# Kernel tuning notes

Measured on AMD Instinct MI355X. Metric: run time of the kernel, lower is better.

The kernel has to match this reference:

```python
import jax, jax.numpy as jnp
import numpy as np

ALPHA = 0.5  # learn_alpha=False -> constant

def _init(key, shape, fan_in):
    return jax.random.normal(key, shape, dtype=jnp.float32) / np.sqrt(fan_in)

def setup_inputs() -> dict:
    key = jax.random.key(0)
    ks = jax.random.split(key, 12)
    B, S, N, F, H, E = 4, 8, 4000, 64, 128, 32000
    x_seq = jax.random.normal(ks[0], (B, S, N, F), dtype=jnp.float32)
    edge_index = jax.random.randint(ks[1], (B, S, 2, E), 0, N, dtype=jnp.int32)
    edge_weight = jax.random.uniform(ks[2], (B, S, E), dtype=jnp.float32)
    params = dict(
        W0_s=_init(ks[3], (H, F), F), b0_s=jnp.zeros((H,), jnp.float32),
        W0_d=_init(ks[4], (H, F), F), b0_d=jnp.zeros((H,), jnp.float32),
        W1_s=_init(ks[5], (H, H), H), b1_s=jnp.zeros((H,), jnp.float32),
        W1_d=_init(ks[6], (H, H), H), b1_d=jnp.zeros((H,), jnp.float32),
        lstm_Wih=_init(ks[7], (4 * H, H), H), lstm_Whh=_init(ks[8], (4 * H, H), H),
        lstm_bih=jnp.zeros((4 * H,), jnp.float32), lstm_bhh=jnp.zeros((4 * H,), jnp.float32),
        Wp=_init(ks[9], (F, H), H), bp=jnp.zeros((F,), jnp.float32),
    )
    return {"x_seq": x_seq, "edge_index": edge_index, "edge_weight": edge_weight, **params}

def _dir_gcn(x, src, dst, ew, Ws, bs, Wd, bd):
    # x: [N, Fin]. DirGCN: alpha * W_s(A_hat x) + (1-alpha) * W_d(A_hat^T x)
    # with symmetric directed normalization D_out^{-1/2} A D_in^{-1/2}.
    N = x.shape[0]
    deg_out = jax.ops.segment_sum(ew, src, num_segments=N)
    deg_in = jax.ops.segment_sum(ew, dst, num_segments=N)
    inv_out = jnp.where(deg_out > 0, jax.lax.rsqrt(jnp.maximum(deg_out, 1e-12)), 0.0)
    inv_in = jnp.where(deg_in > 0, jax.lax.rsqrt(jnp.maximum(deg_in, 1e-12)), 0.0)
    norm = ew * inv_out[src] * inv_in[dst]                         # [E]
    agg_f = jax.ops.segment_sum(norm[:, None] * x[src], dst, num_segments=N)  # A_hat x
    agg_b = jax.ops.segment_sum(norm[:, None] * x[dst], src, num_segments=N)  # A_hat^T x
    return ALPHA * (agg_f @ Ws.T + bs) + (1.0 - ALPHA) * (agg_b @ Wd.T + bd)

def reference(x_seq, edge_index, edge_weight, W0_s, b0_s, W0_d, b0_d,
              W1_s, b1_s, W1_d, b1_d, lstm_Wih, lstm_Whh, lstm_bih, lstm_bhh, Wp, bp):
    B, S, N, F = x_seq.shape
    H = W0_s.shape[0]
    G = B * S
    # fuse the per-(batch, timestep) python loops into one batched graph pass
    x = x_seq.reshape(G, N, F)
    src = edge_index[:, :, 0, :].reshape(G, -1)
    dst = edge_index[:, :, 1, :].reshape(G, -1)
    ew = edge_weight.reshape(G, -1)
    conv = jax.vmap(_dir_gcn, in_axes=(0, 0, 0, 0, None, None, None, None))
    h = conv(x, src, dst, ew, W0_s, b0_s, W0_d, b0_d)   # dropout is a no-op in eval mode
    h = conv(h, src, dst, ew, W1_s, b1_s, W1_d, b1_d)   # [G, N, H]
    # faithful to original: [B, S*N, H].reshape(B*N, S, H) (order-preserving flatten)
    seq = h.reshape(B * N, S, H)
    # single-layer unidirectional LSTM, batch_first; pytorch gate order i,f,g,o
    def step(carry, x_t):
        hprev, c = carry
        gates = x_t @ lstm_Wih.T + lstm_bih + hprev @ lstm_Whh.T + lstm_bhh
        i, f, g, o = jnp.split(gates, 4, axis=-1)
        c = jax.nn.sigmoid(f) * c + jax.nn.sigmoid(i) * jnp.tanh(g)
        hn = jax.nn.sigmoid(o) * jnp.tanh(c)
        return (hn, c), None
    h0 = jnp.zeros((B * N, H), x_seq.dtype)
    (h_last, _), _ = jax.lax.scan(step, (h0, h0), seq.transpose(1, 0, 2))
    return h_last.reshape(B, N, H) @ Wp.T + bp           # [B, N, num_features]
```

## Files before the change

kernel.cpp:

```cpp
#include <hip/hip_runtime.h>
#include <hip/hip_bf16.h>

#define B_  4
#define S_  8
#define N_  4000
#define F_  64
#define H_  128
#define E_  32000
#define G_  (B_*S_)
#define GN_ (G_*N_)
#define M_  (B_*N_)
#define GE_ (G_*E_)
#define HALF_GN 64000
#define HALF_M  8000
#define NBLK_   8
#define EPB_    (E_/NBLK_)

#define OFF_W0S 0
#define OFF_B0S 8192
#define OFF_W0D 8320
#define OFF_B0D 16512
#define OFF_W1S 16640
#define OFF_B1S 33024
#define OFF_W1D 33152
#define OFF_B1D 49536
#define OFF_WIH 49664
#define OFF_WHH 115200
#define OFF_BIH 180736
#define OFF_BHH 181248
#define OFF_WP  181760
#define OFF_BP  189952
#define WCV_TOTAL 190016

#define WS_FLAG   0
#define WS_WCV    16
#define WS_WPH    190032
#define WS_WPC    222800
#define WS_BIASC  288336
#define WS_DEGO   288848
#define WS_DEGI   416848
#define WS_CNTI   544848
#define WS_CNTO   672848
#define WS_RPI    800848
#define WS_RPO    928880
#define WS_CURI   1056912
#define WS_CURO   1184912
#define WS_CSRI   1312912
#define WS_CSRO   3360912
#define WS_X2     5408912
#define WS_PART   9608912
#define WS_HB     21792912
#define WS_GT     29984912
#define WS_WC0    46368912

typedef __attribute__((ext_vector_type(8))) short bf16x8;
typedef __attribute__((ext_vector_type(4))) float f32x4;
typedef __attribute__((ext_vector_type(8))) unsigned short ushort8;

__device__ inline float bfu2f(unsigned short u){ union{unsigned int i; float f;} v; v.i=((unsigned int)u)<<16; return v.f; }
__device__ inline unsigned short f2bfu(float f){ __hip_bfloat16 b = __float2bfloat16(f); return *(unsigned short*)&b; }
__device__ inline float rcpf(float x){ return __builtin_amdgcn_rcpf(x); }
__device__ inline float sigmf(float x){ return rcpf(1.0f + __expf(-x)); }
__device__ inline float tanhfast(float x){ return 1.0f - 2.0f*rcpf(1.0f + __expf(2.0f*x)); }
__device__ inline float loadf(const void* p, long i, int isf32){
    return isf32 ? ((const float*)p)[i]
                 : __bfloat162float(((const __hip_bfloat16*)p)[i]);
}
__device__ inline float4 cvtbf4(ushort4 u){
    float4 f;
    f.x = __uint_as_float(((unsigned)u.x)<<16);
    f.y = __uint_as_float(((unsigned)u.y)<<16);
    f.z = __uint_as_float(((unsigned)u.z)<<16);
    f.w = __uint_as_float(((unsigned)u.w)<<16);
    return f;
}

__global__ void sniff_kernel(const unsigned int* __restrict__ ew, int* __restrict__ flag){
    __shared__ int s;
    if (threadIdx.x == 0) s = 0;
    __syncthreads();
    unsigned int lo = ew[threadIdx.x] & 0xFFFFu;
    if (lo > 0x3F80u) atomicOr(&s, 1);
    __syncthreads();
    if (threadIdx.x == 0) flag[0] = s;
}

struct WSeg { const void* src; int base; int n; };
struct WDesc { WSeg seg[14]; };
__global__ void convert_weights(WDesc d, float* __restrict__ dst, const int* __restrict__ flag){
    int isf32 = flag[0];
    int idx = blockIdx.x*256 + threadIdx.x;
    #pragma unroll
    for (int s=0;s<14;s++){
        int off = idx - d.seg[s].base;
        if (off >= 0 && off < d.seg[s].n){
            dst[idx] = loadf(d.seg[s].src, off, isf32);
            return;
        }
    }
}

__global__ void repack_whh(const float* __restrict__ wcv, unsigned short* __restrict__ whb){
    int idx = blockIdx.x*256 + threadIdx.x;
    whb[idx] = f2bfu(wcv[OFF_WHH + idx]);
}

__global__ void repack_wc0(const float* __restrict__ wcv, unsigned short* __restrict__ wc0){
    int idx = blockIdx.x*256 + threadIdx.x;
    int k = idx & 127, n = idx >> 7;
    float v = (k < 64) ? 0.5f*wcv[OFF_W0S + n*64 + k] : 0.5f*wcv[OFF_W0D + n*64 + (k-64)];
    wc0[idx] = f2bfu(v);
}

__global__ void xcvt_kernel(const void* __restrict__ x, const int* __restrict__ flag,
                            unsigned short* __restrict__ Xb){
    long idx = (long)blockIdx.x*256 + threadIdx.x;
    if (idx >= (long)GN_*64) return;
    Xb[idx] = f2bfu(loadf(x, idx, flag[0]));
}

__global__ __launch_bounds__(256) void compose_wc(const float* __restrict__ wcv,
                                                  unsigned short* __restrict__ wpc){
    int n = blockIdx.x;
    int k = threadIdx.x;
    const float* wih = wcv + OFF_WIH + n*128;
    const float* w1  = (k < 128) ? (wcv + OFF_W1S + k) : (wcv + OFF_W1D + (k-128));
    float s = 0.f;
    for (int h=0; h<128; h++) s += wih[h] * w1[h*128];
    wpc[n*256 + k] = f2bfu(0.5f * s);
}

__global__ void compose_bias(const float* __restrict__ wcv, float* __restrict__ biasc){
    int n = blockIdx.x*256 + threadIdx.x;
    if (n >= 512) return;
    float s = wcv[OFF_BIH+n] + wcv[OFF_BHH+n];
    const float* wih = wcv + OFF_WIH + n*128;
    for (int h=0; h<128; h++) s += wih[h] * 0.5f*(wcv[OFF_B1S+h] + wcv[OFF_B1D+h]);
    biasc[n] = s;
}

__global__ __launch_bounds__(1024) void hist_kernel(
        const int* __restrict__ ei, const void* __restrict__ ew, const int* __restrict__ flag,
        float* __restrict__ part){
    __shared__ float wdo[N_], wdi[N_];
    __shared__ int   co[N_],  ci[N_];
    int xcd  = blockIdx.x & 7;
    int r2   = blockIdx.x >> 3;
    int g    = xcd*4 + (r2 & 3);
    int b    = r2 >> 2;
    int tid  = threadIdx.x;
    int isf32 = flag[0];
    for (int i=tid;i<N_;i+=1024){ wdo[i]=0.f; wdi[i]=0.f; co[i]=0; ci[i]=0; }
    __syncthreads();
    const int* eib = ei + g*2*E_;
    int e0 = b*EPB_;
    for (int e=e0+tid; e<e0+EPB_; e+=1024){
        int s = eib[e], d = eib[E_+e];
        float w = loadf(ew, (long)g*E_+e, isf32);
        atomicAdd(&wdo[s], w); atomicAdd(&wdi[d], w);
        atomicAdd(&co[s], 1);  atomicAdd(&ci[d], 1);
    }
    __syncthreads();
    float* Pdo = part + (size_t)(0*G_ + g)*NBLK_*N_ + (size_t)b*N_;
    float* Pdi = part + (size_t)(1*G_ + g)*NBLK_*N_ + (size_t)b*N_;
    int*   Pci = (int*)part + (size_t)(2*G_ + g)*NBLK_*N_ + (size_t)b*N_;
    int*   Pco = (int*)part + (size_t)(3*G_ + g)*NBLK_*N_ + (size_t)b*N_;
    for (int i=tid;i<N_;i+=1024){
        Pdo[i] = wdo[i]; Pdi[i] = wdi[i];
        Pci[i] = ci[i];  Pco[i] = co[i];
    }
}

__global__ __launch_bounds__(256) void reduce_hist(
        float* __restrict__ part,
        float* __restrict__ deg_o, float* __restrict__ deg_i,
        int* __restrict__ cnt_in, int* __restrict__ cnt_out){
    int g = blockIdx.x >> 4;
    int n = (blockIdx.x & 15)*256 + threadIdx.x;
    if (n >= N_) return;
    float* Pdo = part + (size_t)(0*G_ + g)*NBLK_*N_;
    float* Pdi = part + (size_t)(1*G_ + g)*NBLK_*N_;
    int*   Pci = (int*)part + (size_t)(2*G_ + g)*NBLK_*N_;
    int*   Pco = (int*)part + (size_t)(3*G_ + g)*NBLK_*N_;
    float sdo = 0.f, sdi = 0.f;
    int sci = 0, sco = 0;
    #pragma unroll
    for (int b=0;b<NBLK_;b++){
        size_t idx = (size_t)b*N_ + n;
        sdo += Pdo[idx]; sdi += Pdi[idx];
        int vi = Pci[idx], vo = Pco[idx];
        Pci[idx] = sci;  Pco[idx] = sco;
        sci += vi; sco += vo;
    }
    deg_o[g*N_+n] = sdo; deg_i[g*N_+n] = sdi;
    cnt_in[g*N_+n] = sci; cnt_out[g*N_+n] = sco;
}

__global__ __launch_bounds__(256) void scan_kernel(
        const int* __restrict__ cnt_in, const int* __restrict__ cnt_out,
        int* __restrict__ rp_in, int* __restrict__ rp_out){
    __shared__ int part[256], pref[256];
    int g = blockIdx.x & 31, dir = blockIdx.x >> 5;
    const int* cnt = (dir ? cnt_out : cnt_in) + g*N_;
    int* rp  = (dir ? rp_out  : rp_in)  + g*(N_+1);
    int tid = threadIdx.x, base = tid*16;
    int sum = 0;
    for (int i=0;i<16;i++){ int p = base+i; if (p < N_) sum += cnt[p]; }
    part[tid] = sum;
    __syncthreads();
    if (tid == 0){ int run = 0; for (int j=0;j<256;j++){ pref[j] = run; run += part[j]; } }
    __syncthreads();
    int run = pref[tid];
    for (int i=0;i<16;i++){
        int p = base+i;
        if (p < N_){ rp[p] = run; run += cnt[p]; }
    }
    if (tid == 255) rp[N_] = run;
}

__global__ __launch_bounds__(1024) void fill_kernel(
        const int* __restrict__ ei, const void* __restrict__ ew,
        const int* __restrict__ flag,
        const float* __restrict__ deg_o, const float* __restrict__ deg_i,
        const int* __restrict__ rp_in, const int* __restrict__ rp_out,
        const float* __restrict__ part,
        int2* __restrict__ csr_in, int2* __restrict__ csr_out){
    __shared__ int lci[N_], lco[N_];
    int xcd  = blockIdx.x & 7;
    int r2   = blockIdx.x >> 3;
    int g    = xcd*4 + (r2 & 3);
    int b    = r2 >> 2;
    int tid  = threadIdx.x;
    int isf32 = flag[0];
    for (int i=tid;i<N_;i+=1024){ lci[i]=0; lco[i]=0; }
    __syncthreads();
    const int* eib = ei + g*2*E_;
    const int* cumI = (const int*)part + (size_t)(2*G_ + g)*NBLK_*N_ + (size_t)b*N_;
    const int* cumO = (const int*)part + (size_t)(3*G_ + g)*NBLK_*N_ + (size_t)b*N_;
    const int* rpi = rp_in  + g*(N_+1);
    const int* rpo = rp_out + g*(N_+1);
    int2* ci = csr_in  + (long)g*E_;
    int2* co = csr_out + (long)g*E_;
    int e0 = b*EPB_;
    for (int e=e0+tid; e<e0+EPB_; e+=1024){
        int s = eib[e], d = eib[E_+e];
        float dout = deg_o[g*N_+s], din = deg_i[g*N_+d];
        float io = dout > 0.f ? rsqrtf(fmaxf(dout, 1e-12f)) : 0.f;
        float ii = din  > 0.f ? rsqrtf(fmaxf(din , 1e-12f)) : 0.f;
        float nrm = loadf(ew, (long)g*E_ + e, isf32) * io * ii;
        int li = atomicAdd(&lci[d], 1);
        ci[rpi[d] + cumI[d] + li] = make_int2(s, __float_as_int(nrm));
        int lo = atomicAdd(&lco[s], 1);
        co[rpo[s] + cumO[s] + lo] = make_int2(d, __float_as_int(nrm));
    }
}

__global__ __launch_bounds__(256) void gather64(
        const int* __restrict__ rp_in, const int* __restrict__ rp_out,
        const int2* __restrict__ csr_in, const int2* __restrict__ csr_out,
        const unsigned short* __restrict__ Xb,
        unsigned short* __restrict__ PQ0){
    int xcd  = blockIdx.x & 7;
    int rest = blockIdx.x >> 3;
    int g    = xcd*4 + (rest & 3);
    int chunk= rest >> 2;
    int wave = threadIdx.x >> 6;
    int lane = threadIdx.x & 63;
    int sub  = lane >> 3;
    int li   = lane & 7;
    int wl   = chunk*32 + wave*8 + sub;
    int dir  = wl >= N_;  int n = wl - dir*N_;
    const int*  rp  = (dir ? rp_out : rp_in) + g*(N_+1);
    const int2* csr = (dir ? csr_out : csr_in) + (long)g*E_;
    int pb = rp[n], pe = rp[n+1];
    int plast = max(pe - 1, 0);
    const unsigned short* base = Xb + (size_t)g*N_*64;
    float acc[8];
    #pragma unroll
    for (int j=0;j<8;j++) acc[j] = 0.f;
    for (int p = pb; __any(p < pe); p += 4){
        float w[4]; ushort8 v[4];
        #pragma unroll
        for (int i=0;i<4;i++){
            int pi = p+i;
            int2 ent = csr[min(pi, plast)];
            w[i] = (pi < pe) ? __int_as_float(ent.y) : 0.f;
            v[i] = *(const ushort8*)(base + ent.x*64 + li*8);
        }
        #pragma unroll
        for (int i=0;i<4;i++)
            #pragma unroll
            for (int j=0;j<8;j++)
                acc[j] += w[i]*bfu2f(v[i][j]);
    }
    ushort8 o;
    #pragma unroll
    for (int j=0;j<8;j++) o[j] = f2bfu(acc[j]);
    *(ushort8*)(PQ0 + (size_t)(g*N_+n)*128 + dir*64 + li*8) = o;
}

__global__ __launch_bounds__(256) void gather128(
        const int* __restrict__ rp_in, const int* __restrict__ rp_out,
        const int2* __restrict__ csr_in, const int2* __restrict__ csr_out,
        const unsigned short* __restrict__ hb,
        unsigned short* __restrict__ X2){
    int xcd  = blockIdx.x & 7;
    int rest = blockIdx.x >> 3;
    int g    = xcd*4 + (rest & 3);
    int chunk= rest >> 2;
    int wave = threadIdx.x >> 6;
    int lane = threadIdx.x & 63;
    int sub  = lane >> 4;
    int li   = lane & 15;
    int wl   = chunk*16 + wave*4 + sub;
    int dir  = wl >= N_;  int n = wl - dir*N_;
    const int*  rp  = (dir ? rp_out : rp_in) + g*(N_+1);
    const int2* csr = (dir ? csr_out : csr_in) + (long)g*E_;
    int pb = rp[n], pe = rp[n+1];
    int plast = max(pe - 1, 0);
    const unsigned short* base = hb + (size_t)g*N_*128;
    float acc[8];
    #pragma unroll
    for (int j=0;j<8;j++) acc[j] = 0.f;
    for (int p = pb; __any(p < pe); p += 4){
        float w[4]; ushort8 v[4];
        #pragma unroll
        for (int i=0;i<4;i++){
            int pi = p+i;
            int2 ent = csr[min(pi, plast)];
            w[i] = (pi < pe) ? __int_as_float(ent.y) : 0.f;
            v[i] = *(const ushort8*)(base + ent.x*128 + li*8);
        }
        #pragma unroll
        for (int i=0;i<4;i++)
            #pragma unroll
            for (int j=0;j<8;j++)
                acc[j] += w[i]*bfu2f(v[i][j]);
    }
    ushort8 o;
    #pragma unroll
    for (int j=0;j<8;j++) o[j] = f2bfu(acc[j]);
    *(ushort8*)(X2 + (size_t)(g*N_+n)*256 + dir*128 + li*8) = o;
}

__global__ __launch_bounds__(256) void gemm0(
        const unsigned short* __restrict__ PQ0, const unsigned short* __restrict__ wc0,
        const float* __restrict__ wcv, __hip_bfloat16* __restrict__ Hb){
    __shared__ unsigned short As[2][64*40];
    int tid  = threadIdx.x;
    int wave = tid >> 6, lane = tid & 63;
    int quad = lane >> 4, l16 = lane & 15;
    int nb = blockIdx.x & 1, mb = blockIdx.x >> 1;
    int m0 = mb*64;
    int col = nb*64 + wave*16 + l16;
    bf16x8 bq[4];
    #pragma unroll
    for (int ks=0; ks<4; ks++)
        bq[ks] = *(const bf16x8*)(wc0 + (size_t)col*128 + ks*32 + quad*8);
    f32x4 acc[4];
    #pragma unroll
    for (int t=0;t<4;t++) acc[t] = (f32x4){0.f,0.f,0.f,0.f};
    int srow = tid>>2, sch = tid&3;
    const unsigned short* src_base = PQ0 + (size_t)(m0 + srow)*128 + sch*8;
    *(float4*)(&As[0][srow*40 + sch*8]) = *(const float4*)(src_base);
    __syncthreads();
    for (int ks=0; ks<4; ks++){
        if (ks < 3)
            *(float4*)(&As[(ks+1)&1][srow*40 + sch*8]) = *(const float4*)(src_base + (ks+1)*32);
        const unsigned short* ab = As[ks&1];
        #pragma unroll
        for (int t=0;t<4;t++){
            bf16x8 a = *(const bf16x8*)(ab + (t*16 + l16)*40 + quad*8);
            acc[t] = __builtin_amdgcn_mfma_f32_16x16x32_bf16(a, bq[ks], acc[t], 0, 0, 0);
        }
        __syncthreads();
    }
    float bias = 0.5f*(wcv[OFF_B0S+col] + wcv[OFF_B0D+col]);
    #pragma unroll
    for (int t=0;t<4;t++){
        #pragma unroll
        for (int r=0;r<4;r++){
            int grow = m0 + t*16 + quad*4 + r;
            Hb[(size_t)grow*128 + col] = __float2bfloat16(acc[t][r] + bias);
        }
    }
}

__global__ __launch_bounds__(256) void gemmg(
        const unsigned short* __restrict__ X2, const unsigned short* __restrict__ wpc,
        const float* __restrict__ biasc, unsigned short* __restrict__ gates, int gn_base){
    __shared__ unsigned short As[2][64*40];
    int tid  = threadIdx.x;
    int wave = tid >> 6, lane = tid & 63;
    int quad = lane >> 4, l16 = lane & 15;
    int nb = blockIdx.x & 7, mb = blockIdx.x >> 3;
    int m0 = mb*64;
    int col = nb*64 + wave*16 + l16;
    bf16x8 bq[8];
    #pragma unroll
    for (int ks=0; ks<8; ks++)
        bq[ks] = *(const bf16x8*)(wpc + (size_t)col*256 + ks*32 + quad*8);
    f32x4 acc[4];
    #pragma unroll
    for (int t=0;t<4;t++) acc[t] = (f32x4){0.f,0.f,0.f,0.f};
    int srow = tid>>2, sch = tid&3;
    const unsigned short* src_base = X2 + (size_t)(gn_base + m0 + srow)*256 + sch*8;
    *(float4*)(&As[0][srow*40 + sch*8]) = *(const float4*)(src_base);
    __syncthreads();
    for (int ks=0; ks<8; ks++){
        if (ks < 7)
            *(float4*)(&As[(ks+1)&1][srow*40 + sch*8]) = *(const float4*)(src_base + (ks+1)*32);
        const unsigned short* ab = As[ks&1];
        #pragma unroll
        for (int t=0;t<4;t++){
            bf16x8 a = *(const bf16x8*)(ab + (t*16 + l16)*40 + quad*8);
            acc[t] = __builtin_amdgcn_mfma_f32_16x16x32_bf16(a, bq[ks], acc[t], 0, 0, 0);
        }
        __syncthreads();
    }
    float bc = biasc[col];
    #pragma unroll
    for (int t=0;t<4;t++){
        #pragma unroll
        for (int r=0;r<4;r++){
            int grow = m0 + t*16 + quad*4 + r;
            gates[(size_t)(grow>>3)*4096 + (size_t)col*8 + (grow&7)] = f2bfu(acc[t][r] + bc);
        }
    }
}

__global__ __launch_bounds__(512) void lstm7(
        const unsigned short* __restrict__ gates3, int mbase,
        const unsigned short* __restrict__ whb,
        const float* __restrict__ wcv, const int* __restrict__ flag,
        void* __restrict__ out){
    __shared__ unsigned short hsh[16*136];
    int tid  = threadIdx.x;
    int w    = tid >> 6;
    int lane = tid & 63;
    int quad = lane >> 4, l15 = lane & 15;
    int mlb  = blockIdx.x * 16;
    int m0   = mbase + mlb;
    int isf32 = flag[0];

    ushort8 pg[4][4];
    const unsigned short* gb = gates3 + (size_t)mlb*4096 + (size_t)(w*16 + l15)*8;
    #pragma unroll
    for (int g=0; g<4; g++)
        #pragma unroll
        for (int r=0; r<4; r++)
            pg[g][r] = *(const ushort8*)(gb + (size_t)(quad*4+r)*4096 + (size_t)g*1024);

    bf16x8 bfrag[4][4];
    #pragma unroll
    for (int g=0; g<4; g++)
        #pragma unroll
        for (int kt=0; kt<4; kt++)
            bfrag[g][kt] = *(const bf16x8*)(whb + (size_t)(g*128 + w*16 + l15)*128 + kt*32 + quad*8);

    for (int t=tid; t<16*136; t+=512) hsh[t] = 0;
    f32x4 c = (f32x4){0.f,0.f,0.f,0.f};
    __syncthreads();

    #pragma unroll
    for (int step=0; step<8; step++){
        f32x4 acc[4];
        #pragma unroll
        for (int g=0; g<4; g++)
            #pragma unroll
            for (int r=0; r<4; r++)
                acc[g][r] = bfu2f(pg[g][r][step]);
        #pragma unroll
        for (int kt=0; kt<4; kt++){
            bf16x8 a = *(const bf16x8*)(hsh + l15*136 + kt*32 + quad*8);
            #pragma unroll
            for (int g=0; g<4; g++)
                acc[g] = __builtin_amdgcn_mfma_f32_16x16x32_bf16(a, bfrag[g][kt], acc[g], 0, 0, 0);
        }
        float hnew[4];
        #pragma unroll
        for (int r=0; r<4; r++){
            float gi = sigmf(acc[0][r]), gf = sigmf(acc[1][r]);
            float gg = tanhfast(acc[2][r]), go = sigmf(acc[3][r]);
            float cc = gf*c[r] + gi*gg;
            c[r] = cc;
            hnew[r] = go*tanhfast(cc);
        }
        __syncthreads();
        #pragma unroll
        for (int r=0; r<4; r++)
            hsh[(quad*4+r)*136 + w*16 + l15] = f2bfu(hnew[r]);
        __syncthreads();
    }
    int r  = tid >> 5;
    int q0 = (tid & 31) * 2;
    float p0 = wcv[OFF_BP + q0], p1 = wcv[OFF_BP + q0 + 1];
    for (int k4=0;k4<32;k4++){
        float4 hv = cvtbf4(*(const ushort4*)(hsh + r*136 + k4*4));
        float4 w0 = *(const float4*)(wcv + OFF_WP + q0*128 + k4*4);
        float4 w1 = *(const float4*)(wcv + OFF_WP + (q0+1)*128 + k4*4);
        p0 += w0.x*hv.x + w0.y*hv.y + w0.z*hv.z + w0.w*hv.w;
        p1 += w1.x*hv.x + w1.y*hv.y + w1.z*hv.z + w1.w*hv.w;
    }
    long o = (long)(m0+r)*64 + q0;
    if (isf32){ ((float*)out)[o] = p0; ((float*)out)[o+1] = p1; }
    else { ((__hip_bfloat16*)out)[o] = __float2bfloat16(p0);
           ((__hip_bfloat16*)out)[o+1] = __float2bfloat16(p1); }
}

extern "C" void kernel_launch(void* const* d_in, const int* in_sizes, int n_in,
                              void* d_out, int out_size, void* d_ws, size_t ws_size,
                              hipStream_t stream){
    const void* x_seq      = d_in[0];
    const int*  edge_index = (const int*)d_in[1];
    const void* edge_weight= d_in[2];

    float* ws    = (float*)d_ws;
    int*   flag  = (int*)(ws + WS_FLAG);
    float* wcv   = ws + WS_WCV;
    unsigned short* whb = (unsigned short*)(ws + WS_WPH);
    unsigned short* wpc = (unsigned short*)(ws + WS_WPC);
    unsigned short* wc0 = (unsigned short*)(ws + WS_WC0);
    float* biasc = ws + WS_BIASC;
    float* deg_o = ws + WS_DEGO;
    float* deg_i = ws + WS_DEGI;
    int*   cnt_i = (int*)(ws + WS_CNTI);
    int*   cnt_o = (int*)(ws + WS_CNTO);
    int*   rp_i  = (int*)(ws + WS_RPI);
    int*   rp_o  = (int*)(ws + WS_RPO);
    float* partb = ws + WS_PART;
    int2*  csr_i = (int2*)(ws + WS_CSRI);
    int2*  csr_o = (int2*)(ws + WS_CSRO);
    unsigned short* X2 = (unsigned short*)(ws + WS_X2);
    unsigned short* Xb = X2;
    __hip_bfloat16* Hb = (__hip_bfloat16*)(ws + WS_HB);
    unsigned short* GT = (unsigned short*)(ws + WS_GT);
    unsigned short* PQ0 = GT;

    sniff_kernel<<<1, 256, 0, stream>>>((const unsigned int*)edge_weight, flag);
    WDesc wd;
    wd.seg[0]  = { d_in[3],  OFF_W0S, 8192  };
    wd.seg[1]  = { d_in[4],  OFF_B0S, 128   };
    wd.seg[2]  = { d_in[5],  OFF_W0D, 8192  };
    wd.seg[3]  = { d_in[6],  OFF_B0D, 128   };
    wd.seg[4]  = { d_in[7],  OFF_W1S, 16384 };
    wd.seg[5]  = { d_in[8],  OFF_B1S, 128   };
    wd.seg[6]  = { d_in[9],  OFF_W1D, 16384 };
    wd.seg[7]  = { d_in[10], OFF_B1D, 128   };
    wd.seg[8]  = { d_in[11], OFF_WIH, 65536 };
    wd.seg[9]  = { d_in[12], OFF_WHH, 65536 };
    wd.seg[10] = { d_in[13], OFF_BIH, 512   };
    wd.seg[11] = { d_in[14], OFF_BHH, 512   };
    wd.seg[12] = { d_in[15], OFF_WP,  8192  };
    wd.seg[13] = { d_in[16], OFF_BP,  64    };
    convert_weights<<<(WCV_TOTAL+255)/256, 256, 0, stream>>>(wd, wcv, flag);
    repack_whh<<<256, 256, 0, stream>>>(wcv, whb);
    repack_wc0<<<64, 256, 0, stream>>>(wcv, wc0);
    compose_wc<<<512, 256, 0, stream>>>(wcv, wpc);
    compose_bias<<<2, 256, 0, stream>>>(wcv, biasc);
    xcvt_kernel<<<(GN_*64+255)/256, 256, 0, stream>>>(x_seq, flag, Xb);

    hist_kernel<<<G_*NBLK_, 1024, 0, stream>>>(edge_index, edge_weight, flag, partb);
    reduce_hist<<<G_*16, 256, 0, stream>>>(partb, deg_o, deg_i, cnt_i, cnt_o);
    scan_kernel<<<64, 256, 0, stream>>>(cnt_i, cnt_o, rp_i, rp_o);
    fill_kernel<<<G_*NBLK_, 1024, 0, stream>>>(edge_index, edge_weight, flag,
                                               deg_o, deg_i, rp_i, rp_o, partb, csr_i, csr_o);

    gather64<<<2*G_*N_/32, 256, 0, stream>>>(rp_i, rp_o, csr_i, csr_o, Xb, PQ0);
    gemm0<<<2*(GN_/64), 256, 0, stream>>>(PQ0, wc0, wcv, Hb);

    gather128<<<2*G_*N_/16, 256, 0, stream>>>(rp_i, rp_o, csr_i, csr_o,
                                              (const unsigned short*)Hb, X2);

    gemmg<<<8*(HALF_GN/64), 256, 0, stream>>>(X2, wpc, biasc, GT, 0);
    lstm7<<<HALF_M/16, 512, 0, stream>>>(GT, 0, whb, wcv, flag, d_out);

    gemmg<<<8*(HALF_GN/64), 256, 0, stream>>>(X2, wpc, biasc, GT, HALF_GN);
    lstm7<<<HALF_M/16, 512, 0, stream>>>(GT, HALF_M, whb, wcv, flag, d_out);
}
```

Before: 550.6 us.

## Fuse sparse gathers with following GEMMs via shared-memory tiles

Merges the layer-0 gather and its GEMM into one kernel, and likewise the layer-1 gather and the LSTM input-gate GEMM. Each block aggregates 64 rows for both directions into LDS and then runs MFMA on them directly. This removes the PQ0 and X2 round trips through global memory and two kernel launches. In exchange, each block now serialises gather work before its MFMA phase. The gate kernel recomputes the four column slabs per block with fewer blocks, and load balancing across irregular degrees may suffer.

```diff
diff --git a/kernel.cpp b/kernel.cpp
--- a/kernel.cpp
+++ b/kernel.cpp
@@ -43,8 +43,6 @@
 #define WS_CNTO   672848
 #define WS_RPI    800848
 #define WS_RPO    928880
-#define WS_CURI   1056912
-#define WS_CURO   1184912
 #define WS_CSRI   1312912
 #define WS_CSRO   3360912
 #define WS_X2     5408912
@@ -255,177 +253,163 @@
     }
 }
 
-__global__ __launch_bounds__(256) void gather64(
+__global__ __launch_bounds__(256) void g0fused(
         const int* __restrict__ rp_in, const int* __restrict__ rp_out,
         const int2* __restrict__ csr_in, const int2* __restrict__ csr_out,
-        const unsigned short* __restrict__ Xb,
-        unsigned short* __restrict__ PQ0){
+        const unsigned short* __restrict__ Xb, const unsigned short* __restrict__ wc0,
+        const float* __restrict__ wcv, __hip_bfloat16* __restrict__ Hb){
+    __shared__ unsigned short As[64*136];
     int xcd  = blockIdx.x & 7;
-    int rest = blockIdx.x >> 3;
-    int g    = xcd*4 + (rest & 3);
-    int chunk= rest >> 2;
-    int wave = threadIdx.x >> 6;
-    int lane = threadIdx.x & 63;
-    int sub  = lane >> 3;
-    int li   = lane & 7;
-    int wl   = chunk*32 + wave*8 + sub;
-    int dir  = wl >= N_;  int n = wl - dir*N_;
-    const int*  rp  = (dir ? rp_out : rp_in) + g*(N_+1);
-    const int2* csr = (dir ? csr_out : csr_in) + (long)g*E_;
-    int pb = rp[n], pe = rp[n+1];
-    int plast = max(pe - 1, 0);
-    const unsigned short* base = Xb + (size_t)g*N_*64;
-    float acc[8];
-    #pragma unroll
-    for (int j=0;j<8;j++) acc[j] = 0.f;
-    for (int p = pb; __any(p < pe); p += 4){
-        float w[4]; ushort8 v[4];
-        #pragma unroll
-        for (int i=0;i<4;i++){
-            int pi = p+i;
-            int2 ent = csr[min(pi, plast)];
-            w[i] = (pi < pe) ? __int_as_float(ent.y) : 0.f;
-            v[i] = *(const ushort8*)(base + ent.x*64 + li*8);
+    int tile = blockIdx.x >> 3;
+    int m0   = (xcd*250 + tile)*64;
+    int tid  = threadIdx.x;
+
+    int gid = tid >> 3, li = tid & 7;
+    #pragma unroll
+    for (int t=0; t<4; t++){
+        int task = t*32 + gid;
+        int dir  = task >> 6, r = task & 63;
+        int grow = m0 + r;
+        int g = grow / N_;  int n = grow - g*N_;
+        const int*  rp  = (dir ? rp_out : rp_in) + g*(N_+1);
+        const int2* csr = (dir ? csr_out : csr_in) + (long)g*E_;
+        int pb = rp[n], pe = rp[n+1];
+        int plast = max(pe - 1, 0);
+        const unsigned short* base = Xb + (size_t)g*N_*64;
+        float acc[8];
+        #pragma unroll
+        for (int j=0;j<8;j++) acc[j] = 0.f;
+        for (int p=pb; p<pe; p+=4){
+            float w4[4]; ushort8 v4[4];
+            #pragma unroll
+            for (int i=0;i<4;i++){
+                int pi = p+i;
+                int2 ent = csr[min(pi, plast)];
+                w4[i] = (pi < pe) ? __int_as_float(ent.y) : 0.f;
+                v4[i] = *(const ushort8*)(base + ent.x*64 + li*8);
+            }
+            #pragma unroll
+            for (int i=0;i<4;i++)
+                #pragma unroll
+                for (int j=0;j<8;j++)
+                    acc[j] += w4[i]*bfu2f(v4[i][j]);
         }
-        #pragma unroll
-        for (int i=0;i<4;i++)
-            #pragma unroll
-            for (int j=0;j<8;j++)
-                acc[j] += w[i]*bfu2f(v[i][j]);
-    }
-    ushort8 o;
-    #pragma unroll
-    for (int j=0;j<8;j++) o[j] = f2bfu(acc[j]);
-    *(ushort8*)(PQ0 + (size_t)(g*N_+n)*128 + dir*64 + li*8) = o;
-}
-
-__global__ __launch_bounds__(256) void gather128(
+        ushort8 o;
+        #pragma unroll
+        for (int j=0;j<8;j++) o[j] = f2bfu(acc[j]);
+        *(ushort8*)(&As[r*136 + dir*64 + li*8]) = o;
+    }
+    __syncthreads();
+
+    int wave = tid >> 6, lane = tid & 63;
+    int quad = lane >> 4, l16 = lane & 15;
+    int colb = wave*16 + l16;
+    bf16x8 bq[2][4];
+    f32x4 acc[2][4];
+    #pragma unroll
+    for (int s=0;s<2;s++){
+        #pragma unroll
+        for (int ks=0;ks<4;ks++)
+            bq[s][ks] = *(const bf16x8*)(wc0 + (size_t)(colb + s*64)*128 + ks*32 + quad*8);
+        #pragma unroll
+        for (int t=0;t<4;t++) acc[s][t] = (f32x4){0.f,0.f,0.f,0.f};
+    }
+    #pragma unroll
+    for (int ks=0;ks<4;ks++){
+        #pragma unroll
+        for (int t=0;t<4;t++){
+            bf16x8 a = *(const bf16x8*)(&As[(t*16 + l16)*136 + ks*32 + quad*8]);
+            acc[0][t] = __builtin_amdgcn_mfma_f32_16x16x32_bf16(a, bq[0][ks], acc[0][t], 0, 0, 0);
+            acc[1][t] = __builtin_amdgcn_mfma_f32_16x16x32_bf16(a, bq[1][ks], acc[1][t], 0, 0, 0);
+        }
+    }
+    #pragma unroll
+    for (int s=0;s<2;s++){
+        int col = colb + s*64;
+        float bias = 0.5f*(wcv[OFF_B0S+col] + wcv[OFF_B0D+col]);
+        #pragma unroll
+        for (int t=0;t<4;t++)
+            #pragma unroll
+            for (int r=0;r<4;r++)
+                Hb[(size_t)(m0 + t*16 + quad*4 + r)*128 + col] = __float2bfloat16(acc[s][t][r] + bias);
+    }
+}
+
+__global__ __launch_bounds__(512) void ggfused(
         const int* __restrict__ rp_in, const int* __restrict__ rp_out,
         const int2* __restrict__ csr_in, const int2* __restrict__ csr_out,
         const unsigned short* __restrict__ hb,
-        unsigned short* __restrict__ X2){
+        const unsigned short* __restrict__ wpc, const float* __restrict__ biasc,
+        unsigned short* __restrict__ gates, int gn_base){
+    __shared__ unsigned short As[64*264];
     int xcd  = blockIdx.x & 7;
-    int rest = blockIdx.x >> 3;
-    int g    = xcd*4 + (rest & 3);
-    int chunk= rest >> 2;
-    int wave = threadIdx.x >> 6;
-    int lane = threadIdx.x & 63;
-    int sub  = lane >> 4;
-    int li   = lane & 15;
-    int wl   = chunk*16 + wave*4 + sub;
-    int dir  = wl >= N_;  int n = wl - dir*N_;
-    const int*  rp  = (dir ? rp_out : rp_in) + g*(N_+1);
-    const int2* csr = (dir ? csr_out : csr_in) + (long)g*E_;
-    int pb = rp[n], pe = rp[n+1];
-    int plast = max(pe - 1, 0);
-    const unsigned short* base = hb + (size_t)g*N_*128;
-    float acc[8];
-    #pragma unroll
-    for (int j=0;j<8;j++) acc[j] = 0.f;
-    for (int p = pb; __any(p < pe); p += 4){
-        float w[4]; ushort8 v[4];
-        #pragma unroll
-        for (int i=0;i<4;i++){
-            int pi = p+i;
-            int2 ent = csr[min(pi, plast)];
-            w[i] = (pi < pe) ? __int_as_float(ent.y) : 0.f;
-            v[i] = *(const ushort8*)(base + ent.x*128 + li*8);
+    int tile = blockIdx.x >> 3;
+    int m0   = (xcd*125 + tile)*64;
+    int tid  = threadIdx.x;
+
+    int gid = tid >> 4, li = tid & 15;
+    #pragma unroll
+    for (int t=0; t<4; t++){
+        int task = t*32 + gid;
+        int dir  = task >> 6, r = task & 63;
+        int grow = gn_base + m0 + r;
+        int g = grow / N_;  int n = grow - g*N_;
+        const int*  rp  = (dir ? rp_out : rp_in) + g*(N_+1);
+        const int2* csr = (dir ? csr_out : csr_in) + (long)g*E_;
+        int pb = rp[n], pe = rp[n+1];
+        int plast = max(pe - 1, 0);
+        const unsigned short* base = hb + (size_t)g*N_*128;
+        float acc[8];
+        #pragma unroll
+        for (int j=0;j<8;j++) acc[j] = 0.f;
+        for (int p=pb; p<pe; p+=4){
+            float w4[4]; ushort8 v4[4];
+            #pragma unroll
+            for (int i=0;i<4;i++){
+                int pi = p+i;
+                int2 ent = csr[min(pi, plast)];
+                w4[i] = (pi < pe) ? __int_as_float(ent.y) : 0.f;
+                v4[i] = *(const ushort8*)(base + ent.x*128 + li*8);
+            }
+            #pragma unroll
+            for (int i=0;i<4;i++)
+                #pragma unroll
+                for (int j=0;j<8;j++)
+                    acc[j] += w4[i]*bfu2f(v4[i][j]);
         }
-        #pragma unroll
-        for (int i=0;i<4;i++)
-            #pragma unroll
-            for (int j=0;j<8;j++)
-                acc[j] += w[i]*bfu2f(v[i][j]);
-    }
-    ushort8 o;
-    #pragma unroll
-    for (int j=0;j<8;j++) o[j] = f2bfu(acc[j]);
-    *(ushort8*)(X2 + (size_t)(g*N_+n)*256 + dir*128 + li*8) = o;
-}
-
-__global__ __launch_bounds__(256) void gemm0(
-        const unsigned short* __restrict__ PQ0, const unsigned short* __restrict__ wc0,
-        const float* __restrict__ wcv, __hip_bfloat16* __restrict__ Hb){
-    __shared__ unsigned short As[2][64*40];
-    int tid  = threadIdx.x;
-    int wave = tid >> 6, lane = tid & 63;
+        ushort8 o;
+        #pragma unroll
+        for (int j=0;j<8;j++) o[j] = f2bfu(acc[j]);
+        *(ushort8*)(&As[r*264 + dir*128 + li*8]) = o;
+    }
+    __syncthreads();
+
+    int w = tid >> 6, lane = tid & 63;
     int quad = lane >> 4, l16 = lane & 15;
-    int nb = blockIdx.x & 1, mb = blockIdx.x >> 1;
-    int m0 = mb*64;
-    int col = nb*64 + wave*16 + l16;
-    bf16x8 bq[4];
-    #pragma unroll
-    for (int ks=0; ks<4; ks++)
-        bq[ks] = *(const bf16x8*)(wc0 + (size_t)col*128 + ks*32 + quad*8);
-    f32x4 acc[4];
-    #pragma unroll
-    for (int t=0;t<4;t++) acc[t] = (f32x4){0.f,0.f,0.f,0.f};
-    int srow = tid>>2, sch = tid&3;
-    const unsigned short* src_base = PQ0 + (size_t)(m0 + srow)*128 + sch*8;
-    *(float4*)(&As[0][srow*40 + sch*8]) = *(const float4*)(src_base);
-    __syncthreads();
-    for (int ks=0; ks<4; ks++){
-        if (ks < 3)
-            *(float4*)(&As[(ks+1)&1][srow*40 + sch*8]) = *(const float4*)(src_base + (ks+1)*32);
-        const unsigned short* ab = As[ks&1];
-        #pragma unroll
-        for (int t=0;t<4;t++){
-            bf16x8 a = *(const bf16x8*)(ab + (t*16 + l16)*40 + quad*8);
-            acc[t] = __builtin_amdgcn_mfma_f32_16x16x32_bf16(a, bq[ks], acc[t], 0, 0, 0);
-        }
-        __syncthreads();
-    }
-    float bias = 0.5f*(wcv[OFF_B0S+col] + wcv[OFF_B0D+col]);
-    #pragma unroll
-    for (int t=0;t<4;t++){
-        #pragma unroll
-        for (int r=0;r<4;r++){
-            int grow = m0 + t*16 + quad*4 + r;
-            Hb[(size_t)grow*128 + col] = __float2bfloat16(acc[t][r] + bias);
-        }
-    }
-}
-
-__global__ __launch_bounds__(256) void gemmg(
-        const unsigned short* __restrict__ X2, const unsigned short* __restrict__ wpc,
-        const float* __restrict__ biasc, unsigned short* __restrict__ gates, int gn_base){
-    __shared__ unsigned short As[2][64*40];
-    int tid  = threadIdx.x;
-    int wave = tid >> 6, lane = tid & 63;
-    int quad = lane >> 4, l16 = lane & 15;
-    int nb = blockIdx.x & 7, mb = blockIdx.x >> 3;
-    int m0 = mb*64;
-    int col = nb*64 + wave*16 + l16;
-    bf16x8 bq[8];
-    #pragma unroll
-    for (int ks=0; ks<8; ks++)
-        bq[ks] = *(const bf16x8*)(wpc + (size_t)col*256 + ks*32 + quad*8);
-    f32x4 acc[4];
-    #pragma unroll
-    for (int t=0;t<4;t++) acc[t] = (f32x4){0.f,0.f,0.f,0.f};
-    int srow = tid>>2, sch = tid&3;
-    const unsigned short* src_base = X2 + (size_t)(gn_base + m0 + srow)*256 + sch*8;
-    *(float4*)(&As[0][srow*40 + sch*8]) = *(const float4*)(src_base);
-    __syncthreads();
-    for (int ks=0; ks<8; ks++){
-        if (ks < 7)
-            *(float4*)(&As[(ks+1)&1][srow*40 + sch*8]) = *(const float4*)(src_base + (ks+1)*32);
-        const unsigned short* ab = As[ks&1];
-        #pragma unroll
-        for (int t=0;t<4;t++){
-            bf16x8 a = *(const bf16x8*)(ab + (t*16 + l16)*40 + quad*8);
-            acc[t] = __builtin_amdgcn_mfma_f32_16x16x32_bf16(a, bq[ks], acc[t], 0, 0, 0);
-        }
-        __syncthreads();
-    }
-    float bc = biasc[col];
-    #pragma unroll
-    for (int t=0;t<4;t++){
-        #pragma unroll
-        for (int r=0;r<4;r++){
-            int grow = m0 + t*16 + quad*4 + r;
-            gates[(size_t)(grow>>3)*4096 + (size_t)col*8 + (grow&7)] = f2bfu(acc[t][r] + bc);
-        }
+    for (int cs=0; cs<4; cs++){
+        int col = cs*128 + w*16 + l16;
+        bf16x8 bq[8];
+        #pragma unroll
+        for (int ks=0;ks<8;ks++)
+            bq[ks] = *(const bf16x8*)(wpc + (size_t)col*256 + ks*32 + quad*8);
+        f32x4 acc[4];
+        #pragma unroll
+        for (int t=0;t<4;t++) acc[t] = (f32x4){0.f,0.f,0.f,0.f};
+        #pragma unroll
+        for (int ks=0;ks<8;ks++)
+            #pragma unroll
+            for (int t=0;t<4;t++){
+                bf16x8 a = *(const bf16x8*)(&As[(t*16 + l16)*264 + ks*32 + quad*8]);
+                acc[t] = __builtin_amdgcn_mfma_f32_16x16x32_bf16(a, bq[ks], acc[t], 0, 0, 0);
+            }
+        float bc = biasc[col];
+        #pragma unroll
+        for (int t=0;t<4;t++)
+            #pragma unroll
+            for (int r=0;r<4;r++){
+                int grow = m0 + t*16 + quad*4 + r;
+                gates[(size_t)(grow>>3)*4096 + (size_t)col*8 + (grow&7)] = f2bfu(acc[t][r] + bc);
+            }
     }
 }
 
@@ -531,11 +515,9 @@
     float* partb = ws + WS_PART;
     int2*  csr_i = (int2*)(ws + WS_CSRI);
     int2*  csr_o = (int2*)(ws + WS_CSRO);
-    unsigned short* X2 = (unsigned short*)(ws + WS_X2);
-    unsigned short* Xb = X2;
+    unsigned short* Xb = (unsigned short*)(ws + WS_X2);
     __hip_bfloat16* Hb = (__hip_bfloat16*)(ws + WS_HB);
     unsigned short* GT = (unsigned short*)(ws + WS_GT);
-    unsigned short* PQ0 = GT;
 
     sniff_kernel<<<1, 256, 0, stream>>>((const unsigned int*)edge_weight, flag);
     WDesc wd;
@@ -566,15 +548,13 @@
     fill_kernel<<<G_*NBLK_, 1024, 0, stream>>>(edge_index, edge_weight, flag,
                                                deg_o, deg_i, rp_i, rp_o, partb, csr_i, csr_o);
 
-    gather64<<<2*G_*N_/32, 256, 0, stream>>>(rp_i, rp_o, csr_i, csr_o, Xb, PQ0);
-    gemm0<<<2*(GN_/64), 256, 0, stream>>>(PQ0, wc0, wcv, Hb);
-
-    gather128<<<2*G_*N_/16, 256, 0, stream>>>(rp_i, rp_o, csr_i, csr_o,
-                                              (const unsigned short*)Hb, X2);
-
-    gemmg<<<8*(HALF_GN/64), 256, 0, stream>>>(X2, wpc, biasc, GT, 0);
+    g0fused<<<GN_/64, 256, 0, stream>>>(rp_i, rp_o, csr_i, csr_o, Xb, wc0, wcv, Hb);
+
+    ggfused<<<HALF_GN/64, 512, 0, stream>>>(rp_i, rp_o, csr_i, csr_o,
+                                            (const unsigned short*)Hb, wpc, biasc, GT, 0);
     lstm7<<<HALF_M/16, 512, 0, stream>>>(GT, 0, whb, wcv, flag, d_out);
 
-    gemmg<<<8*(HALF_GN/64), 256, 0, stream>>>(X2, wpc, biasc, GT, HALF_GN);
+    ggfused<<<HALF_GN/64, 512, 0, stream>>>(rp_i, rp_o, csr_i, csr_o,
+                                            (const unsigned short*)Hb, wpc, biasc, GT, HALF_GN);
     lstm7<<<HALF_M/16, 512, 0, stream>>>(GT, HALF_M, whb, wcv, flag, d_out);
 }
```

After: 513.3 us. -6.8%, faster.
